# Performance work log

Measured on AMD Instinct MI355X. Metric: run time of the kernel, lower is better.

The kernel has to match this reference:

```python
import jax, jax.numpy as jnp
import numpy as np

T = 16384       # video length (frames)
C = 7           # out_features = d_model = num surgical phases
F_DIM = 2048    # mstcn_f_dim (spatial feature dim)
LEN_Q = 30      # sliding window length
N_HEADS = 4
D_K = 64        # attn_dim = min(64, mstcn_f_maps=64)
D_FF = 64       # d_ff = mstcn_f_maps


def setup_inputs() -> dict:
    key = jax.random.key(0)
    ks = jax.random.split(key, 10)
    w = lambda i, shape: jax.random.normal(ks[i], shape, jnp.float32) * 0.05
    return {
        "x": jax.random.normal(ks[0], (1, C, T), jnp.float32),
        "long_feature": jax.random.normal(ks[1], (1, T, F_DIM), jnp.float32),
        "W_fc": w(2, (C, F_DIM)),              # nn.Linear(mstcn_f_dim, out_features, bias=False)
        "W_q": w(3, (N_HEADS * D_K, C)),
        "W_k": w(4, (N_HEADS * D_K, C)),
        "W_v": w(5, (N_HEADS * D_K, C)),
        "W_o": w(6, (C, N_HEADS * D_K)),
        "ln1_g": jnp.ones((C,), jnp.float32),
        "ln1_b": jnp.zeros((C,), jnp.float32),
        "W_ff1": w(7, (D_FF, C)),
        "W_ff2": w(8, (C, D_FF)),
        "ln2_g": jnp.ones((C,), jnp.float32),
        "ln2_b": jnp.zeros((C,), jnp.float32),
    }


def layer_norm(x, g, b, eps=1e-5):
    mu = x.mean(-1, keepdims=True)
    var = ((x - mu) ** 2).mean(-1, keepdims=True)
    return (x - mu) * jax.lax.rsqrt(var + eps) * g + b


def reference(x, long_feature, W_fc, W_q, W_k, W_v, W_o, ln1_g, ln1_b, W_ff1, W_ff2, ln2_g, ln2_b):
    # --- vectorized sliding-window (replaces the Python loop of zeros/cat/stack) ---
    feats = x[0].T                                            # (T, C)
    padded = jnp.concatenate([jnp.zeros((LEN_Q - 1, C), feats.dtype), feats], axis=0)
    idx = jnp.arange(T)[:, None] + jnp.arange(LEN_Q)[None, :]  # window ends at frame i
    inputs = padded[idx]                                       # (T, LEN_Q, C)

    # --- spatial embedding: feas = tanh(fc(long_feature)).transpose(0,1) ---
    feas = jnp.tanh(long_feature[0] @ W_fc.T)[:, None, :]      # (T, 1, C)

    # --- decoder layer: cross MHA(query=feas, kv=inputs) + residual + LN ---
    q = (feas @ W_q.T).reshape(T, 1, N_HEADS, D_K).transpose(0, 2, 1, 3)       # (T,H,1,Dk)
    k = (inputs @ W_k.T).reshape(T, LEN_Q, N_HEADS, D_K).transpose(0, 2, 1, 3)  # (T,H,Lq,Dk)
    v = (inputs @ W_v.T).reshape(T, LEN_Q, N_HEADS, D_K).transpose(0, 2, 1, 3)  # (T,H,Lq,Dk)
    scores = jnp.einsum('thqd,thkd->thqk', q, k) / np.float32(np.sqrt(D_K))
    attn = jax.nn.softmax(scores, axis=-1)
    ctx = jnp.einsum('thqk,thkd->thqd', attn, v)
    ctx = ctx.transpose(0, 2, 1, 3).reshape(T, 1, N_HEADS * D_K)
    out = layer_norm(ctx @ W_o.T + feas, ln1_g, ln1_b)         # (T, 1, C)

    # --- position-wise FFN + residual + LN ---
    ff = jax.nn.relu(out @ W_ff1.T) @ W_ff2.T
    out = layer_norm(ff + out, ln2_g, ln2_b)
    return out[:, 0]                                           # (T, C) per-frame logits
```

## Files before the change

kernel.cpp:

```cpp
#include <hip/hip_runtime.h>
#include <math.h>

#define T_FRAMES 16384
#define FDIM 2048
#define LQ 30
#define FPB 8

__global__ __launch_bounds__(448) void setup_kernel(
    const float* __restrict__ Wq, const float* __restrict__ Wk,
    const float* __restrict__ Wv, const float* __restrict__ Wo,
    float* __restrict__ AM) {
  const int e = threadIdx.x;
  if (e >= 392) return;
  const int which = e / 196;
  const int r = e % 196;
  const int h = r / 49;
  const int rr = r % 49;
  const int c = rr / 7;
  const int c2 = rr % 7;
  float s = 0.0f;
  if (which == 0) {
    for (int d = 0; d < 64; ++d)
      s = fmaf(Wq[(h * 64 + d) * 7 + c], Wk[(h * 64 + d) * 7 + c2], s);
  } else {
    for (int d = 0; d < 64; ++d)
      s = fmaf(Wo[c * 256 + h * 64 + d], Wv[(h * 64 + d) * 7 + c2], s);
  }
  AM[e] = s;
}

__global__ __launch_bounds__(256) void fused_kernel(
    const float* __restrict__ lf,
    const float* __restrict__ Wfc,
    const float* __restrict__ x,
    const float* __restrict__ AM,
    const float* __restrict__ W1,
    const float* __restrict__ W2,
    const float* __restrict__ ln1g, const float* __restrict__ ln1b,
    const float* __restrict__ ln2g, const float* __restrict__ ln2b,
    float* __restrict__ out) {
  __shared__ float feas_s[FPB][7];
  __shared__ float AM_s[392];
  __shared__ float ft[(FPB + LQ - 1) * 7];
  __shared__ float hpart[FPB][4][7];

  const int tid = threadIdx.x;
  const int lane = tid & 63;
  const int wave = tid >> 6;
  const int t0 = blockIdx.x * FPB;

  for (int i = tid; i < 392; i += 256) AM_s[i] = AM[i];
  for (int i = tid; i < (FPB + LQ - 1) * 7; i += 256) {
    const int row = i / 7, c = i % 7;
    const int s = t0 - (LQ - 1) + row;
    ft[i] = (s >= 0) ? x[c * T_FRAMES + s] : 0.0f;
  }

  const int tf = t0 + wave * 2;
  const float* lfp0 = lf + (size_t)tf * FDIM;
  const float* lfp1 = lfp0 + FDIM;
  const int fl = lane * 4;

  float acc0[7], acc1[7];
#pragma unroll
  for (int c = 0; c < 7; ++c) { acc0[c] = 0.0f; acc1[c] = 0.0f; }

  for (int chunk = 0; chunk < 8; ++chunk) {
    const int f = chunk * 256 + fl;
    const float4 a0 = *(const float4*)(lfp0 + f);
    const float4 a1 = *(const float4*)(lfp1 + f);
#pragma unroll
    for (int c = 0; c < 7; ++c) {
      const float4 w = *(const float4*)(Wfc + c * FDIM + f);
      acc0[c] = fmaf(a0.x, w.x, fmaf(a0.y, w.y, fmaf(a0.z, w.z, fmaf(a0.w, w.w, acc0[c]))));
      acc1[c] = fmaf(a1.x, w.x, fmaf(a1.y, w.y, fmaf(a1.z, w.z, fmaf(a1.w, w.w, acc1[c]))));
    }
  }

#pragma unroll
  for (int c = 0; c < 7; ++c) {
    float v0 = acc0[c], v1 = acc1[c];
    for (int off = 32; off > 0; off >>= 1) {
      v0 += __shfl_down(v0, off, 64);
      v1 += __shfl_down(v1, off, 64);
    }
    if (lane == 0) {
      feas_s[wave * 2 + 0][c] = tanhf(v0);
      feas_s[wave * 2 + 1][c] = tanhf(v1);
    }
  }
  __syncthreads();

  if (tid < FPB * 4) {
    const int f = tid >> 2;
    const int h = tid & 3;
    float fe[7];
#pragma unroll
    for (int c = 0; c < 7; ++c) fe[c] = feas_s[f][c];

    const float* Ah = AM_s + h * 49;
    const float* Mh = AM_s + 196 + h * 49;
    float qk[7];
#pragma unroll
    for (int c2 = 0; c2 < 7; ++c2) {
      float s = 0.0f;
#pragma unroll
      for (int c = 0; c < 7; ++c) s = fmaf(fe[c], Ah[c * 7 + c2], s);
      qk[c2] = s * 0.125f;
    }
    const float* frow = &ft[f * 7];
    float sc[LQ];
    float m = -1e30f;
#pragma unroll
    for (int j = 0; j < LQ; ++j) {
      const float* r = frow + j * 7;
      float s = 0.0f;
#pragma unroll
      for (int c2 = 0; c2 < 7; ++c2) s = fmaf(qk[c2], r[c2], s);
      sc[j] = s;
      m = fmaxf(m, s);
    }
    float sum = 0.0f;
    float wsum[7] = {0, 0, 0, 0, 0, 0, 0};
#pragma unroll
    for (int j = 0; j < LQ; ++j) {
      const float p = __expf(sc[j] - m);
      sum += p;
      const float* r = frow + j * 7;
#pragma unroll
      for (int c2 = 0; c2 < 7; ++c2) wsum[c2] = fmaf(p, r[c2], wsum[c2]);
    }
    const float inv = 1.0f / sum;
#pragma unroll
    for (int c = 0; c < 7; ++c) {
      float s = 0.0f;
#pragma unroll
      for (int c2 = 0; c2 < 7; ++c2) s = fmaf(Mh[c * 7 + c2], wsum[c2], s);
      hpart[f][h][c] = s * inv;
    }
  }
  __syncthreads();

  if (tid < FPB) {
    const int f = tid;
    float v[7];
#pragma unroll
    for (int c = 0; c < 7; ++c)
      v[c] = feas_s[f][c] + hpart[f][0][c] + hpart[f][1][c] + hpart[f][2][c] + hpart[f][3][c];

    float mu = 0.0f;
#pragma unroll
    for (int c = 0; c < 7; ++c) mu += v[c];
    mu *= (1.0f / 7.0f);
    float var = 0.0f;
#pragma unroll
    for (int c = 0; c < 7; ++c) { const float d = v[c] - mu; var = fmaf(d, d, var); }
    var *= (1.0f / 7.0f);
    float rs = rsqrtf(var + 1e-5f);
    float o1[7];
#pragma unroll
    for (int c = 0; c < 7; ++c) o1[c] = (v[c] - mu) * rs * ln1g[c] + ln1b[c];

    float ff[7] = {0, 0, 0, 0, 0, 0, 0};
    for (int k = 0; k < 64; ++k) {
      float hk = 0.0f;
#pragma unroll
      for (int c = 0; c < 7; ++c) hk = fmaf(W1[k * 7 + c], o1[c], hk);
      hk = fmaxf(hk, 0.0f);
#pragma unroll
      for (int c = 0; c < 7; ++c) ff[c] = fmaf(W2[c * 64 + k], hk, ff[c]);
    }

#pragma unroll
    for (int c = 0; c < 7; ++c) v[c] = ff[c] + o1[c];
    mu = 0.0f;
#pragma unroll
    for (int c = 0; c < 7; ++c) mu += v[c];
    mu *= (1.0f / 7.0f);
    var = 0.0f;
#pragma unroll
    for (int c = 0; c < 7; ++c) { const float d = v[c] - mu; var = fmaf(d, d, var); }
    var *= (1.0f / 7.0f);
    rs = rsqrtf(var + 1e-5f);
    const int t = t0 + f;
#pragma unroll
    for (int c = 0; c < 7; ++c)
      out[(size_t)t * 7 + c] = (v[c] - mu) * rs * ln2g[c] + ln2b[c];
  }
}

extern "C" void kernel_launch(void* const* d_in, const int* in_sizes, int n_in,
                              void* d_out, int out_size, void* d_ws, size_t ws_size,
                              hipStream_t stream) {
  const float* x    = (const float*)d_in[0];
  const float* lf   = (const float*)d_in[1];
  const float* Wfc  = (const float*)d_in[2];
  const float* Wq   = (const float*)d_in[3];
  const float* Wk   = (const float*)d_in[4];
  const float* Wv   = (const float*)d_in[5];
  const float* Wo   = (const float*)d_in[6];
  const float* ln1g = (const float*)d_in[7];
  const float* ln1b = (const float*)d_in[8];
  const float* W1   = (const float*)d_in[9];
  const float* W2   = (const float*)d_in[10];
  const float* ln2g = (const float*)d_in[11];
  const float* ln2b = (const float*)d_in[12];
  float* out = (float*)d_out;

  float* AM = (float*)d_ws;

  setup_kernel<<<1, 448, 0, stream>>>(Wq, Wk, Wv, Wo, AM);
  fused_kernel<<<T_FRAMES / FPB, 256, 0, stream>>>(
      lf, Wfc, x, AM, W1, W2, ln1g, ln1b, ln2g, ln2b, out);
}
```

Measured before the change: 267.1 us.

## Stage W_fc in shared memory, enlarge blocks, prefetch feature chunks

Each block now copies the full 7x2048 W_fc matrix into LDS (56 KB) and uses 1024 threads covering 32 frames instead of 256 threads covering 8. The projection loop software-prefetches the next long_feature chunk into registers, and the attention matrices are read straight from global instead of staged in LDS. The goal is fewer redundant global/L2 reads of W_fc and more latency hiding on the streaming 128 MB feature read. In exchange, each block pays a 56 KB LDS fill that only 32 frames reuse, and occupancy is limited by the large LDS footprint.

```diff
diff --git a/kernel.cpp b/kernel.cpp
--- a/kernel.cpp
+++ b/kernel.cpp
@@ -4,7 +4,9 @@
 #define T_FRAMES 16384
 #define FDIM 2048
 #define LQ 30
-#define FPB 8
+#define FPB 32
+#define NTHR 1024
+#define FPW 2
 
 __global__ __launch_bounds__(448) void setup_kernel(
     const float* __restrict__ Wq, const float* __restrict__ Wk,
@@ -29,7 +31,7 @@
   AM[e] = s;
 }
 
-__global__ __launch_bounds__(256) void fused_kernel(
+__global__ __launch_bounds__(NTHR) void fused_kernel(
     const float* __restrict__ lf,
     const float* __restrict__ Wfc,
     const float* __restrict__ x,
@@ -39,9 +41,9 @@
     const float* __restrict__ ln1g, const float* __restrict__ ln1b,
     const float* __restrict__ ln2g, const float* __restrict__ ln2b,
     float* __restrict__ out) {
+  __shared__ float wfc_s[7 * FDIM];
+  __shared__ float ft[(FPB + LQ - 1) * 7];
   __shared__ float feas_s[FPB][7];
-  __shared__ float AM_s[392];
-  __shared__ float ft[(FPB + LQ - 1) * 7];
   __shared__ float hpart[FPB][4][7];
 
   const int tid = threadIdx.x;
@@ -49,14 +51,19 @@
   const int wave = tid >> 6;
   const int t0 = blockIdx.x * FPB;
 
-  for (int i = tid; i < 392; i += 256) AM_s[i] = AM[i];
-  for (int i = tid; i < (FPB + LQ - 1) * 7; i += 256) {
+  {
+    const float4* wsrc = (const float4*)Wfc;
+    float4* wdst = (float4*)wfc_s;
+    for (int i = tid; i < 7 * (FDIM / 4); i += NTHR) wdst[i] = wsrc[i];
+  }
+  for (int i = tid; i < (FPB + LQ - 1) * 7; i += NTHR) {
     const int row = i / 7, c = i % 7;
     const int s = t0 - (LQ - 1) + row;
     ft[i] = (s >= 0) ? x[c * T_FRAMES + s] : 0.0f;
   }
-
-  const int tf = t0 + wave * 2;
+  __syncthreads();
+
+  const int tf = t0 + wave * FPW;
   const float* lfp0 = lf + (size_t)tf * FDIM;
   const float* lfp1 = lfp0 + FDIM;
   const int fl = lane * 4;
@@ -65,16 +72,24 @@
 #pragma unroll
   for (int c = 0; c < 7; ++c) { acc0[c] = 0.0f; acc1[c] = 0.0f; }
 
+  float4 c0 = *(const float4*)(lfp0 + fl);
+  float4 c1 = *(const float4*)(lfp1 + fl);
+#pragma unroll
   for (int chunk = 0; chunk < 8; ++chunk) {
+    float4 n0, n1;
+    if (chunk < 7) {
+      const int fn = (chunk + 1) * 256 + fl;
+      n0 = *(const float4*)(lfp0 + fn);
+      n1 = *(const float4*)(lfp1 + fn);
+    }
     const int f = chunk * 256 + fl;
-    const float4 a0 = *(const float4*)(lfp0 + f);
-    const float4 a1 = *(const float4*)(lfp1 + f);
 #pragma unroll
     for (int c = 0; c < 7; ++c) {
-      const float4 w = *(const float4*)(Wfc + c * FDIM + f);
-      acc0[c] = fmaf(a0.x, w.x, fmaf(a0.y, w.y, fmaf(a0.z, w.z, fmaf(a0.w, w.w, acc0[c]))));
-      acc1[c] = fmaf(a1.x, w.x, fmaf(a1.y, w.y, fmaf(a1.z, w.z, fmaf(a1.w, w.w, acc1[c]))));
-    }
+      const float4 w = *(const float4*)(&wfc_s[c * FDIM + f]);
+      acc0[c] = fmaf(c0.x, w.x, fmaf(c0.y, w.y, fmaf(c0.z, w.z, fmaf(c0.w, w.w, acc0[c]))));
+      acc1[c] = fmaf(c1.x, w.x, fmaf(c1.y, w.y, fmaf(c1.z, w.z, fmaf(c1.w, w.w, acc1[c]))));
+    }
+    if (chunk < 7) { c0 = n0; c1 = n1; }
   }
 
 #pragma unroll
@@ -85,8 +100,8 @@
       v1 += __shfl_down(v1, off, 64);
     }
     if (lane == 0) {
-      feas_s[wave * 2 + 0][c] = tanhf(v0);
-      feas_s[wave * 2 + 1][c] = tanhf(v1);
+      feas_s[wave * FPW + 0][c] = tanhf(v0);
+      feas_s[wave * FPW + 1][c] = tanhf(v1);
     }
   }
   __syncthreads();
@@ -98,8 +113,8 @@
 #pragma unroll
     for (int c = 0; c < 7; ++c) fe[c] = feas_s[f][c];
 
-    const float* Ah = AM_s + h * 49;
-    const float* Mh = AM_s + 196 + h * 49;
+    const float* Ah = AM + h * 49;
+    const float* Mh = AM + 196 + h * 49;
     float qk[7];
 #pragma unroll
     for (int c2 = 0; c2 < 7; ++c2) {
@@ -210,6 +225,6 @@
   float* AM = (float*)d_ws;
 
   setup_kernel<<<1, 448, 0, stream>>>(Wq, Wk, Wv, Wo, AM);
-  fused_kernel<<<T_FRAMES / FPB, 256, 0, stream>>>(
+  fused_kernel<<<T_FRAMES / FPB, NTHR, 0, stream>>>(
       lf, Wfc, x, AM, W1, W2, ln1g, ln1b, ln2g, ln2b, out);
 }
```

Measured after the change: 397.8 us. +48.9%, slower.
